# Kernel tuning notes

Hardware: AMD Instinct MI355X
Metric: run time of the kernel (lower is better)

## Reference

```python
import jax, jax.numpy as jnp
import numpy as np

B = 4096          # batch
F = 1024          # feature_count * embedding_dim
E = 16            # embedding_dim (domain embedding)
D = 8             # num_domains
T = F + E         # cross-net total dim
L = 3             # cross layers
EPS = 1e-5


def setup_inputs() -> dict:
    key = jax.random.key(0)
    ks = jax.random.split(key, 32)
    s = 0.02
    inp = {}
    inp["x"] = jax.random.normal(ks[0], (B, F), dtype=jnp.float32)
    inp["domain_ids"] = jax.random.randint(ks[1], (B,), 0, D)
    # partitioned normalization params
    inp["pn_weight"] = jnp.ones((D, F), jnp.float32)
    inp["pn_bias"] = jnp.zeros((D, F), jnp.float32)
    # domain embedding table
    inp["dom_emb"] = jax.random.normal(ks[2], (D, E), jnp.float32) * 0.1
    # cross network: L layers, each Linear(T->1, no bias) + additive bias vector
    inp["cross_w"] = jax.random.normal(ks[3], (L, T), jnp.float32) * s
    inp["cross_b"] = jnp.zeros((L, T), jnp.float32)
    # center MLP: T->512->256->128 (ReLU, ReLU, none)
    inp["cW1"] = jax.random.normal(ks[4], (T, 512), jnp.float32) * s
    inp["cb1"] = jnp.zeros((512,), jnp.float32)
    inp["cW2"] = jax.random.normal(ks[5], (512, 256), jnp.float32) * s
    inp["cb2"] = jnp.zeros((256,), jnp.float32)
    inp["cW3"] = jax.random.normal(ks[6], (256, 128), jnp.float32) * s
    inp["cb3"] = jnp.zeros((128,), jnp.float32)
    # per-domain nets: T->512->256->128; last bias initialized to domain_net_init_bias=1.0
    inp["dW1"] = jax.random.normal(ks[7], (D, T, 512), jnp.float32) * s
    inp["db1"] = jnp.zeros((D, 512), jnp.float32)
    inp["dW2"] = jax.random.normal(ks[8], (D, 512, 256), jnp.float32) * s
    inp["db2"] = jnp.zeros((D, 256), jnp.float32)
    inp["dW3"] = jax.random.normal(ks[9], (D, 256, 128), jnp.float32) * s
    inp["db3"] = jnp.ones((D, 128), jnp.float32)
    # final MLP: 128->64->1
    inp["fW1"] = jax.random.normal(ks[10], (128, 64), jnp.float32) * s
    inp["fb1"] = jnp.zeros((64,), jnp.float32)
    inp["fW2"] = jax.random.normal(ks[11], (64, 1), jnp.float32) * s
    inp["fb2"] = jnp.zeros((1,), jnp.float32)
    # auxiliary net: E->32->1
    inp["aW1"] = jax.random.normal(ks[12], (E, 32), jnp.float32) * s
    inp["ab1"] = jnp.zeros((32,), jnp.float32)
    inp["aW2"] = jax.random.normal(ks[13], (32, 1), jnp.float32) * s
    inp["ab2"] = jnp.zeros((1,), jnp.float32)
    return inp


def _forward(x, domain_ids, pn_weight, pn_bias, dom_emb, cross_w, cross_b,
             cW1, cb1, cW2, cb2, cW3, cb3,
             dW1, db1, dW2, db2, dW3, db3,
             fW1, fb1, fW2, fb2, aW1, ab1, aW2, ab2):
    # --- PartitionedNormalization: per-sample LayerNorm stats + domain-indexed affine ---
    mean = jnp.mean(x, axis=1, keepdims=True)
    var = jnp.mean((x - mean) ** 2, axis=1, keepdims=True)  # unbiased=False
    normed = (x - mean) / jnp.sqrt(var + EPS)
    normed = normed * pn_weight[domain_ids] + pn_bias[domain_ids]

    xd = dom_emb[domain_ids]                    # (B, E)
    x0 = jnp.concatenate([normed, xd], axis=1)  # (B, T)

    # --- CrossNetworkWithDomain ---
    xc = x0
    for i in range(L):
        proj = xc @ cross_w[i]                  # (B,)
        xc = x0 * proj[:, None] + cross_b[i] + xc

    # --- center MLP ---
    h = jax.nn.relu(xc @ cW1 + cb1)
    h = jax.nn.relu(h @ cW2 + cb2)
    h_center = h @ cW3 + cb3                    # (B, 128)

    # --- domain-specific nets: run all D nets, select per-sample ---
    a = jax.nn.relu(jnp.einsum('bi,dio->bdo', xc, dW1) + db1[None])   # (B, D, 512)
    a = jax.nn.relu(jnp.einsum('bdi,dio->bdo', a, dW2) + db2[None])   # (B, D, 256)
    a = jnp.einsum('bdi,dio->bdo', a, dW3) + db3[None]                # (B, D, 128)
    h_domain = a[jnp.arange(a.shape[0]), domain_ids]                  # (B, 128)

    # --- STAR fusion (tanh) ---
    fused = h_center * jnp.tanh(h_domain)

    # --- final MLP + auxiliary net ---
    main_logits = jax.nn.relu(fused @ fW1 + fb1) @ fW2 + fb2          # (B, 1)
    aux_logits = jax.nn.relu(xd @ aW1 + ab1) @ aW2 + ab2              # (B, 1)
    return jax.nn.sigmoid(main_logits + aux_logits)


def reference(x, domain_ids, pn_weight, pn_bias, dom_emb, cross_w, cross_b,
              cW1, cb1, cW2, cb2, cW3, cb3,
              dW1, db1, dW2, db2, dW3, db3,
              fW1, fb1, fW2, fb2, aW1, ab1, aW2, ab2):
    return _forward(x, domain_ids, pn_weight, pn_bias, dom_emb, cross_w, cross_b,
                    cW1, cb1, cW2, cb2, cW3, cb3,
                    dW1, db1, dW2, db2, dW3, db3,
                    fW1, fb1, fW2, fb2, aW1, ab1, aW2, ab2)
```

## Files before the change

### kernel.cpp

```cpp
#include <hip/hip_runtime.h>
#include <math.h>
#include <stdint.h>

#define BATCH 4096
#define FEAT  1024
#define EDIM  16
#define NDOM  8
#define TDIM  1040
#define KP1   1088
#define NLAYER 3
#define EPSV  1e-5f

typedef __attribute__((ext_vector_type(8))) short bf16x8;
typedef __attribute__((ext_vector_type(4))) float f32x4;

#define VMW(N)  __builtin_amdgcn_s_waitcnt((((N)&15)|(((N)>>4)<<14)|(15<<8)|(7<<4)))
#define LGKW0   __builtin_amdgcn_s_waitcnt((15|(3<<14)|(7<<4)))
#define SBAR    __builtin_amdgcn_s_barrier()
#define SCB     __builtin_amdgcn_sched_barrier(0)

__device__ __forceinline__ unsigned short f2bf(float f) {
    union { float f; unsigned int u; } v; v.f = f;
    unsigned int u = v.u;
    return (unsigned short)((u + 0x7fffu + ((u >> 16) & 1u)) >> 16);
}
__device__ __forceinline__ float bf2f(unsigned short u) {
    union { unsigned int u; float f; } v; v.u = ((unsigned int)u) << 16; return v.f;
}
__device__ __forceinline__ void gload_lds16(const void* g, void* l) {
    __builtin_amdgcn_global_load_lds(
        (const __attribute__((address_space(1))) void*)(g),
        (__attribute__((address_space(3))) void*)(l), 16, 0, 0);
}

#define T_W1 136
#define T_W2 32
#define T_W3 8
#define NCONV (T_W1*9 + T_W2*9 + T_W3*9)

__global__ __launch_bounds__(256) void front(
    const int* __restrict__ dom, int* __restrict__ perm, int* __restrict__ starts,
    const float* __restrict__ cW1, const float* __restrict__ dW1,
    const float* __restrict__ cW2, const float* __restrict__ dW2,
    const float* __restrict__ cW3, const float* __restrict__ dW3,
    unsigned short* __restrict__ Wc1b, unsigned short* __restrict__ Wd1b,
    unsigned short* __restrict__ Wc2b, unsigned short* __restrict__ Wd2b,
    unsigned short* __restrict__ Wc3b, unsigned short* __restrict__ Wd3b,
    const float* __restrict__ x,
    const float* __restrict__ pnw, const float* __restrict__ pnb,
    const float* __restrict__ demb,
    const float* __restrict__ crw, const float* __restrict__ crb,
    const float* __restrict__ aW1, const float* __restrict__ ab1,
    const float* __restrict__ aW2, const float* __restrict__ ab2,
    unsigned short* __restrict__ XCb, float* __restrict__ auxg) {
    int b = blockIdx.x;
    int t = threadIdx.x;

    if (b < NCONV) {
        __shared__ float tile[64][65];
        const float* src; unsigned short* dst; int K, N, Kp, rr;
        if (b < T_W1)            { src = cW1; dst = Wc1b; K = TDIM; N = 512; Kp = KP1; rr = b; }
        else if (b < T_W1*9)     { int r = b - T_W1; int z = r / T_W1; rr = r % T_W1;
                                   src = dW1 + (size_t)z * TDIM * 512; dst = Wd1b + (size_t)z * 512 * KP1;
                                   K = TDIM; N = 512; Kp = KP1; }
        else if (b < T_W1*9+T_W2)   { src = cW2; dst = Wc2b; K = 512; N = 256; Kp = 512; rr = b - T_W1*9; }
        else if (b < T_W1*9+T_W2*9) { int r = b - (T_W1*9+T_W2); int z = r / T_W2; rr = r % T_W2;
                                   src = dW2 + (size_t)z * 512 * 256; dst = Wd2b + (size_t)z * 256 * 512;
                                   K = 512; N = 256; Kp = 512; }
        else if (b < T_W1*9+T_W2*9+T_W3) { src = cW3; dst = Wc3b; K = 256; N = 128; Kp = 256; rr = b - (T_W1*9+T_W2*9); }
        else                     { int r = b - (T_W1*9+T_W2*9+T_W3); int z = r / T_W3; rr = r % T_W3;
                                   src = dW3 + (size_t)z * 256 * 128; dst = Wd3b + (size_t)z * 128 * 256;
                                   K = 256; N = 128; Kp = 256; }
        int kt = Kp >> 6;
        int kb = rr % kt, nb = rr / kt;
        int k0 = kb * 64, n0 = nb * 64;
        #pragma unroll
        for (int i = 0; i < 4; i++) {
            int flat = t + i * 256;
            int kr = flat >> 4, c4 = flat & 15;
            int k = k0 + kr;
            float4 v = make_float4(0.f, 0.f, 0.f, 0.f);
            if (k < K) v = *(const float4*)(src + (size_t)k * N + n0 + c4 * 4);
            tile[kr][c4 * 4 + 0] = v.x;
            tile[kr][c4 * 4 + 1] = v.y;
            tile[kr][c4 * 4 + 2] = v.z;
            tile[kr][c4 * 4 + 3] = v.w;
        }
        __syncthreads();
        #pragma unroll
        for (int i = 0; i < 4; i++) {
            int flat = t + i * 256;
            int n = flat >> 4, kg = flat & 15;
            ushort4 sv;
            sv.x = f2bf(tile[kg * 4 + 0][n]);
            sv.y = f2bf(tile[kg * 4 + 1][n]);
            sv.z = f2bf(tile[kg * 4 + 2][n]);
            sv.w = f2bf(tile[kg * 4 + 3][n]);
            *(ushort4*)(dst + (size_t)(n0 + n) * Kp + k0 + kg * 4) = sv;
        }
        return;
    }
    if (b == NCONV) {
        __shared__ int cnt[NDOM];
        __shared__ int off[NDOM];
        if (t < NDOM) cnt[t] = 0;
        __syncthreads();
        for (int i = t; i < BATCH; i += 256) atomicAdd(&cnt[dom[i]], 1);
        __syncthreads();
        if (t == 0) {
            int s = 0;
            for (int d = 0; d < NDOM; d++) { off[d] = s; starts[d] = s; s += cnt[d]; }
            starts[NDOM] = s;
        }
        __syncthreads();
        for (int i = t; i < BATCH; i += 256) {
            int p = atomicAdd(&off[dom[i]], 1);
            perm[p] = i;
        }
        return;
    }

    int w = t >> 6, lane = t & 63;
    int row = (b - NCONV - 1) * 4 + w;
    int d = dom[row];

    float4 X[4];
    #pragma unroll
    for (int j = 0; j < 4; j++)
        X[j] = *(const float4*)(x + (size_t)row * FEAT + 4 * lane + 256 * j);

    float s = 0.f, ss = 0.f;
    #pragma unroll
    for (int j = 0; j < 4; j++) {
        s  += X[j].x + X[j].y + X[j].z + X[j].w;
        ss += X[j].x*X[j].x + X[j].y*X[j].y + X[j].z*X[j].z + X[j].w*X[j].w;
    }
    #pragma unroll
    for (int m = 1; m < 64; m <<= 1) {
        s  += __shfl_xor(s,  m);
        ss += __shfl_xor(ss, m);
    }
    float mean = s / (float)FEAT;
    float var  = ss / (float)FEAT - mean * mean;
    float rstd = rsqrtf(var + EPSV);

    float4 x0[4], xc[4];
    #pragma unroll
    for (int j = 0; j < 4; j++) {
        float4 wv = *(const float4*)(pnw + (size_t)d * FEAT + 4 * lane + 256 * j);
        float4 bv = *(const float4*)(pnb + (size_t)d * FEAT + 4 * lane + 256 * j);
        x0[j].x = (X[j].x - mean) * rstd * wv.x + bv.x;
        x0[j].y = (X[j].y - mean) * rstd * wv.y + bv.y;
        x0[j].z = (X[j].z - mean) * rstd * wv.z + bv.z;
        x0[j].w = (X[j].w - mean) * rstd * wv.w + bv.w;
        xc[j] = x0[j];
    }
    float x0e = 0.f, xce = 0.f;
    if (lane < EDIM) { x0e = demb[d * EDIM + lane]; xce = x0e; }

    #pragma unroll
    for (int l = 0; l < NLAYER; l++) {
        const float* wl = crw + l * TDIM;
        const float* bl = crb + l * TDIM;
        float partial = 0.f;
        #pragma unroll
        for (int j = 0; j < 4; j++) {
            float4 wv = *(const float4*)(wl + 4 * lane + 256 * j);
            partial += xc[j].x*wv.x + xc[j].y*wv.y + xc[j].z*wv.z + xc[j].w*wv.w;
        }
        if (lane < EDIM) partial += xce * wl[FEAT + lane];
        #pragma unroll
        for (int m = 1; m < 64; m <<= 1) partial += __shfl_xor(partial, m);
        float proj = partial;
        #pragma unroll
        for (int j = 0; j < 4; j++) {
            float4 bv = *(const float4*)(bl + 4 * lane + 256 * j);
            xc[j].x = fmaf(x0[j].x, proj, bv.x + xc[j].x);
            xc[j].y = fmaf(x0[j].y, proj, bv.y + xc[j].y);
            xc[j].z = fmaf(x0[j].z, proj, bv.z + xc[j].z);
            xc[j].w = fmaf(x0[j].w, proj, bv.w + xc[j].w);
        }
        if (lane < EDIM) xce = fmaf(x0e, proj, bl[FEAT + lane] + xce);
    }

    #pragma unroll
    for (int j = 0; j < 4; j++) {
        ushort4 sv;
        sv.x = f2bf(xc[j].x); sv.y = f2bf(xc[j].y);
        sv.z = f2bf(xc[j].z); sv.w = f2bf(xc[j].w);
        *(ushort4*)(XCb + (size_t)row * KP1 + 4 * lane + 256 * j) = sv;
    }
    XCb[(size_t)row * KP1 + FEAT + lane] = (lane < EDIM) ? f2bf(xce) : 0;

    float h = (lane < 32) ? ab1[lane] : 0.f;
    #pragma unroll
    for (int e = 0; e < EDIM; e++) {
        float ev = __shfl(xce, e);
        if (lane < 32) h = fmaf(ev, aW1[e * 32 + lane], h);
    }
    float c = (lane < 32) ? fmaxf(h, 0.f) * aW2[lane] : 0.f;
    #pragma unroll
    for (int m = 1; m < 64; m <<= 1) c += __shfl_xor(c, m);
    if (lane == 0) auxg[row] = c + ab2[0];
}

__global__ __launch_bounds__(256) void gemm_l1_fused(
    const unsigned short* __restrict__ A,
    const unsigned short* __restrict__ Wc,
    const unsigned short* __restrict__ Wd,
    const float* __restrict__ bc, const float* __restrict__ bd,
    unsigned short* __restrict__ Cc, unsigned short* __restrict__ Cd,
    const int* __restrict__ starts, const int* __restrict__ perm) {
    __shared__ short As[2][64 * 64];
    __shared__ short Bs[2][128 * 64];

    int g = blockIdx.x;
    int d = 0, acc = 0, m0 = -1, mEnd = 0;
    #pragma unroll
    for (int dd = 0; dd < NDOM; dd++) {
        int c0 = starts[dd], c1 = starts[dd + 1];
        int ns = (c1 - c0 + 63) >> 6;
        if (m0 < 0 && g < acc + ns) { d = dd; m0 = c0 + ((g - acc) << 6); mEnd = c1; }
        acc += ns;
    }
    if (m0 < 0) return;
    int n0 = blockIdx.y * 64;

    int tid = threadIdx.x;
    int w = tid >> 6, lane = tid & 63;
    int lr = lane & 15, q = lane >> 4;

    const unsigned short* pA[2]; int sA[2];
    const unsigned short* pB[4]; int sB[4];
    #pragma unroll
    for (int i = 0; i < 2; i++) {
        int seg = i * 4 + w;
        int ch = seg * 64 + lane;
        int loc = ch >> 3, c = ch & 7;
        int mm = m0 + loc; if (mm > mEnd - 1) mm = mEnd - 1;
        int rowp = perm[mm];
        pA[i] = A + (size_t)rowp * KP1 + ((c ^ (loc & 7)) << 3);
        sA[i] = seg * 512;
    }
    #pragma unroll
    for (int i = 0; i < 4; i++) {
        int seg = i * 4 + w;
        int ch = seg * 64 + lane;
        int loc = ch >> 3, c = ch & 7;
        const unsigned short* base = (loc < 64)
            ? (Wc + (size_t)(n0 + loc) * KP1)
            : (Wd + ((size_t)d * 512 + n0 + (loc - 64)) * KP1);
        pB[i] = base + ((c ^ (loc & 7)) << 3);
        sB[i] = seg * 512;
    }

    f32x4 acc4[4][2];
    #pragma unroll
    for (int i = 0; i < 4; i++)
        #pragma unroll
        for (int j = 0; j < 2; j++)
            acc4[i][j] = (f32x4){0.f, 0.f, 0.f, 0.f};

    #pragma unroll
    for (int i = 0; i < 2; i++) gload_lds16(pA[i], As[0] + sA[i]);
    #pragma unroll
    for (int i = 0; i < 4; i++) gload_lds16(pB[i], Bs[0] + sB[i]);

    #pragma unroll 1
    for (int ks = 0; ks < KP1 / 64; ks++) {
        int cur = ks & 1, nxt = cur ^ 1;
        if (ks < KP1 / 64 - 1) {
            int k0 = (ks + 1) * 64;
            #pragma unroll
            for (int i = 0; i < 2; i++) gload_lds16(pA[i] + k0, As[nxt] + sA[i]);
            #pragma unroll
            for (int i = 0; i < 4; i++) gload_lds16(pB[i] + k0, Bs[nxt] + sB[i]);
            VMW(6);
        } else {
            VMW(0);
        }
        SBAR; SCB;
        #pragma unroll
        for (int half = 0; half < 2; half++) {
            int cc = half * 4 + q;
            bf16x8 af[4], bf[2];
            #pragma unroll
            for (int i = 0; i < 4; i++) {
                int m = i * 16 + lr;
                af[i] = *(const bf16x8*)(As[cur] + m * 64 + ((cc ^ (m & 7)) << 3));
            }
            #pragma unroll
            for (int j = 0; j < 2; j++) {
                int n = w * 32 + j * 16 + lr;
                bf[j] = *(const bf16x8*)(Bs[cur] + n * 64 + ((cc ^ (n & 7)) << 3));
            }
            #pragma unroll
            for (int i = 0; i < 4; i++)
                #pragma unroll
                for (int j = 0; j < 2; j++)
                    acc4[i][j] = __builtin_amdgcn_mfma_f32_16x16x32_bf16(
                        af[i], bf[j], acc4[i][j], 0, 0, 0);
        }
        LGKW0; SBAR; SCB;
    }

    int chain = w >> 1, hn = w & 1;
    const float* bias = chain ? (bd + d * 512) : bc;
    unsigned short* C = chain ? Cd : Cc;
    #pragma unroll
    for (int i = 0; i < 4; i++) {
        #pragma unroll
        for (int j = 0; j < 2; j++) {
            int col = n0 + hn * 32 + j * 16 + lr;
            float bvv = bias[col];
            int rowb = m0 + i * 16 + q * 4;
            #pragma unroll
            for (int r = 0; r < 4; r++) {
                int row = rowb + r;
                if (row >= mEnd) continue;
                C[(size_t)row * 512 + col] = f2bf(fmaxf(acc4[i][j][r] + bvv, 0.f));
            }
        }
    }
}

__global__ __launch_bounds__(256) void tail_fused(
    const unsigned short* __restrict__ H1c, const unsigned short* __restrict__ H1d,
    const unsigned short* __restrict__ Wc2, const unsigned short* __restrict__ Wd2,
    const float* __restrict__ cb2v, const float* __restrict__ db2v,
    const unsigned short* __restrict__ Wc3, const unsigned short* __restrict__ Wd3,
    const float* __restrict__ cb3v, const float* __restrict__ db3v,
    const float* __restrict__ fW1, const float* __restrict__ fb1,
    const float* __restrict__ fW2, const float* __restrict__ fb2,
    const float* __restrict__ auxg, const int* __restrict__ perm,
    const int* __restrict__ starts, float* __restrict__ out) {

    __shared__ __align__(16) char smem[98304];
    short* BufB[2]; short* BufA[2];
    #pragma unroll
    for (int i = 0; i < 2; i++) {
        BufB[i] = (short*)(smem + i * 36864);
        BufA[i] = (short*)(smem + i * 36864 + 32768);
    }
    short* H2    = (short*)(smem + 73728);
    short* fused = (short*)(smem + 90112);

    int g = blockIdx.x;
    int d = 0, acc = 0, m0 = -1, mEnd = 0;
    #pragma unroll
    for (int dd = 0; dd < NDOM; dd++) {
        int c0 = starts[dd], c1 = starts[dd + 1];
        int ns = (c1 - c0 + 31) >> 5;
        if (m0 < 0 && g < acc + ns) { d = dd; m0 = c0 + ((g - acc) << 5); mEnd = c1; }
        acc += ns;
    }
    if (m0 < 0) return;

    int tid = threadIdx.x;
    int w = tid >> 6, lane = tid & 63;
    int lr = lane & 15, q = lane >> 4;

    int bn = w * 8 + (lane >> 3);
    int sw = ((lane & 7) ^ (bn & 7)) << 3;
    int rowA = m0 + bn; if (rowA > mEnd - 1) rowA = mEnd - 1;

    const unsigned short* pA0  = H1c + (size_t)rowA * 512 + sw;
    const unsigned short* pA1  = H1d + (size_t)rowA * 512 + sw;
    const unsigned short* pW20 = Wc2 + (size_t)bn * 512 + sw;
    const unsigned short* pW21 = Wd2 + (size_t)d * 256 * 512 + (size_t)bn * 512 + sw;
    const unsigned short* pW30 = Wc3 + (size_t)bn * 256 + sw;
    const unsigned short* pW31 = Wd3 + (size_t)d * 128 * 256 + (size_t)bn * 256 + sw;

    auto istep = [&](int s) {
        int c = s / 12, k = s % 12, b = s & 1;
        if (k < 8) {
            const unsigned short* pa = c ? pA1 : pA0;
            const unsigned short* pw = c ? pW21 : pW20;
            int k0 = k * 64;
            gload_lds16(pa + k0, BufA[b] + w * 512);
            #pragma unroll
            for (int i = 0; i < 8; i++)
                gload_lds16(pw + (size_t)i * 32 * 512 + k0, BufB[b] + (i * 4 + w) * 512);
        } else {
            const unsigned short* pw = c ? pW31 : pW30;
            int k0 = (k - 8) * 64;
            #pragma unroll
            for (int i = 0; i < 4; i++)
                gload_lds16(pw + (size_t)i * 32 * 256 + k0, BufB[b] + (i * 4 + w) * 512);
        }
    };

    f32x4 acc2[2][4], acc3[2][2];

    auto cstep = [&](int s) {
        int c = s / 12, k = s % 12, b = s & 1;
        if (k < 8) {
            if (k == 0) {
                #pragma unroll
                for (int i = 0; i < 2; i++)
                    #pragma unroll
                    for (int j = 0; j < 4; j++) acc2[i][j] = (f32x4){0.f, 0.f, 0.f, 0.f};
            }
            #pragma unroll
            for (int half = 0; half < 2; half++) {
                int cc = half * 4 + q;
                bf16x8 af[2], bf[4];
                #pragma unroll
                for (int i = 0; i < 2; i++) {
                    int m = i * 16 + lr;
                    af[i] = *(const bf16x8*)(BufA[b] + m * 64 + ((cc ^ (m & 7)) << 3));
                }
                #pragma unroll
                for (int j = 0; j < 4; j++) {
                    int n = w * 64 + j * 16 + lr;
                    bf[j] = *(const bf16x8*)(BufB[b] + n * 64 + ((cc ^ (n & 7)) << 3));
                }
                #pragma unroll
                for (int i = 0; i < 2; i++)
                    #pragma unroll
                    for (int j = 0; j < 4; j++)
                        acc2[i][j] = __builtin_amdgcn_mfma_f32_16x16x32_bf16(
                            af[i], bf[j], acc2[i][j], 0, 0, 0);
            }
            if (k == 7) {
                const float* b2 = c ? (db2v + d * 256) : cb2v;
                #pragma unroll
                for (int i = 0; i < 2; i++)
                    #pragma unroll
                    for (int j = 0; j < 4; j++) {
                        int col = w * 64 + j * 16 + lr;
                        float bv = b2[col];
                        int cch = col >> 3;
                        #pragma unroll
                        for (int r = 0; r < 4; r++) {
                            int row = i * 16 + q * 4 + r;
                            int pc = (cch & 24) | ((cch ^ (row & 7)) & 7);
                            float v = fmaxf(acc2[i][j][r] + bv, 0.f);
                            H2[row * 256 + pc * 8 + (col & 7)] = (short)f2bf(v);
                        }
                    }
            }
        } else {
            int it = k - 8;
            if (it == 0) {
                #pragma unroll
                for (int i = 0; i < 2; i++)
                    #pragma unroll
                    for (int j = 0; j < 2; j++) acc3[i][j] = (f32x4){0.f, 0.f, 0.f, 0.f};
            }
            #pragma unroll
            for (int half = 0; half < 2; half++) {
                int cc = half * 4 + q;
                int C = it * 8 + cc;
                bf16x8 af[2], bf[2];
                #pragma unroll
                for (int i = 0; i < 2; i++) {
                    int m = i * 16 + lr;
                    int pcm = (C & 24) | ((C ^ (m & 7)) & 7);
                    af[i] = *(const bf16x8*)(H2 + m * 256 + pcm * 8);
                }
                #pragma unroll
                for (int j = 0; j < 2; j++) {
                    int n = w * 32 + j * 16 + lr;
                    bf[j] = *(const bf16x8*)(BufB[b] + n * 64 + ((cc ^ (n & 7)) << 3));
                }
                #pragma unroll
                for (int i = 0; i < 2; i++)
                    #pragma unroll
                    for (int j = 0; j < 2; j++)
                        acc3[i][j] = __builtin_amdgcn_mfma_f32_16x16x32_bf16(
                            af[i], bf[j], acc3[i][j], 0, 0, 0);
            }
            if (it == 3) {
                const float* b3 = c ? (db3v + d * 128) : cb3v;
                #pragma unroll
                for (int i = 0; i < 2; i++)
                    #pragma unroll
                    for (int j = 0; j < 2; j++) {
                        int col = w * 32 + j * 16 + lr;
                        float bv = b3[col];
                        int cch = col >> 3;
                        #pragma unroll
                        for (int r = 0; r < 4; r++) {
                            int row = i * 16 + q * 4 + r;
                            int pc = (cch & 8) | ((cch ^ (row & 7)) & 7);
                            int idx = row * 128 + pc * 8 + (col & 7);
                            if (c == 0) {
                                fused[idx] = (short)f2bf(acc3[i][j][r] + bv);
                            } else {
                                float cv = bf2f((unsigned short)fused[idx]);
                                fused[idx] = (short)f2bf(cv * tanhf(acc3[i][j][r] + bv));
                            }
                        }
                    }
            }
        }
    };

    #define TSTEP(S, NW) do { \
        VMW(NW); SBAR; SCB; \
        cstep(S); \
        LGKW0; SBAR; SCB; \
        if ((S) + 2 < 24) istep((S) + 2); \
    } while (0)

    istep(0); istep(1);

    TSTEP(0, 9);   TSTEP(1, 9);   TSTEP(2, 9);   TSTEP(3, 9);
    TSTEP(4, 9);   TSTEP(5, 9);   TSTEP(6, 9);   TSTEP(7, 4);
    TSTEP(8, 4);   TSTEP(9, 4);   TSTEP(10, 4);  TSTEP(11, 9);
    TSTEP(12, 9);  TSTEP(13, 9);  TSTEP(14, 9);  TSTEP(15, 9);
    TSTEP(16, 9);  TSTEP(17, 9);  TSTEP(18, 9);  TSTEP(19, 4);
    TSTEP(20, 4);  TSTEP(21, 4);  TSTEP(22, 4);  TSTEP(23, 0);
    #undef TSTEP

    __syncthreads();

    short* Bsf = BufB[0];
    float* Ls  = (float*)BufA[0];
    for (int s2 = tid; s2 < 1024; s2 += 256) {
        int n = s2 >> 4, cch = s2 & 15;
        bf16x8 vv;
        #pragma unroll
        for (int kk = 0; kk < 8; kk++)
            vv[kk] = (short)f2bf(fW1[(cch * 8 + kk) * 64 + n]);
        int pc = (cch & 8) | ((cch ^ (n & 7)) & 7);
        *(bf16x8*)(Bsf + n * 128 + pc * 8) = vv;
    }
    __syncthreads();

    int wm = w >> 1, wn = w & 1;
    f32x4 acc2f[2];
    #pragma unroll
    for (int j = 0; j < 2; j++) acc2f[j] = (f32x4){0.f, 0.f, 0.f, 0.f};
    #pragma unroll
    for (int g2 = 0; g2 < 4; g2++) {
        int cc = g2 * 4 + q;
        int m = wm * 16 + lr;
        int pcm = (cc & 8) | ((cc ^ (m & 7)) & 7);
        bf16x8 af = *(const bf16x8*)(fused + m * 128 + pcm * 8);
        #pragma unroll
        for (int j = 0; j < 2; j++) {
            int n = wn * 32 + j * 16 + lr;
            int pcn = (cc & 8) | ((cc ^ (n & 7)) & 7);
            bf16x8 bf = *(const bf16x8*)(Bsf + n * 128 + pcn * 8);
            acc2f[j] = __builtin_amdgcn_mfma_f32_16x16x32_bf16(af, bf, acc2f[j], 0, 0, 0);
        }
    }

    float w2v[2], b1v[2];
    #pragma unroll
    for (int j = 0; j < 2; j++) {
        int col = wn * 32 + j * 16 + lr;
        w2v[j] = fW2[col];
        b1v[j] = fb1[col];
    }
    float rowv[4];
    #pragma unroll
    for (int r = 0; r < 4; r++) {
        float v = 0.f;
        #pragma unroll
        for (int j = 0; j < 2; j++)
            v += fmaxf(acc2f[j][r] + b1v[j], 0.f) * w2v[j];
        v += __shfl_xor(v, 1);
        v += __shfl_xor(v, 2);
        v += __shfl_xor(v, 4);
        v += __shfl_xor(v, 8);
        rowv[r] = v;
    }
    if (wn == 0 && lr == 0) {
        #pragma unroll
        for (int r = 0; r < 4; r++)
            Ls[wm * 16 + q * 4 + r] = rowv[r];
    }
    __syncthreads();
    if (wn == 1 && lr == 0) {
        float b2 = fb2[0];
        #pragma unroll
        for (int r = 0; r < 4; r++) {
            int row = wm * 16 + q * 4 + r;
            int p = m0 + row;
            if (p < mEnd) {
                int orow = perm[p];
                float logit = Ls[row] + rowv[r] + b2 + auxg[orow];
                out[orow] = 1.f / (1.f + expf(-logit));
            }
        }
    }
}

extern "C" void kernel_launch(void* const* d_in, const int* in_sizes, int n_in,
                              void* d_out, int out_size, void* d_ws, size_t ws_size,
                              hipStream_t stream) {
    (void)in_sizes; (void)n_in; (void)out_size; (void)ws_size;

    const float* x    = (const float*)d_in[0];
    const int*   dom  = (const int*)  d_in[1];
    const float* pnw  = (const float*)d_in[2];
    const float* pnb  = (const float*)d_in[3];
    const float* demb = (const float*)d_in[4];
    const float* crw  = (const float*)d_in[5];
    const float* crb  = (const float*)d_in[6];
    const float* cW1  = (const float*)d_in[7];
    const float* cb1  = (const float*)d_in[8];
    const float* cW2  = (const float*)d_in[9];
    const float* cb2  = (const float*)d_in[10];
    const float* cW3  = (const float*)d_in[11];
    const float* cb3  = (const float*)d_in[12];
    const float* dW1  = (const float*)d_in[13];
    const float* db1  = (const float*)d_in[14];
    const float* dW2  = (const float*)d_in[15];
    const float* db2  = (const float*)d_in[16];
    const float* dW3  = (const float*)d_in[17];
    const float* db3  = (const float*)d_in[18];
    const float* fW1  = (const float*)d_in[19];
    const float* fb1  = (const float*)d_in[20];
    const float* fW2  = (const float*)d_in[21];
    const float* fb2  = (const float*)d_in[22];
    const float* aW1  = (const float*)d_in[23];
    const float* ab1  = (const float*)d_in[24];
    const float* aW2  = (const float*)d_in[25];
    const float* ab2  = (const float*)d_in[26];
    float* out = (float*)d_out;

    char* base = (char*)d_ws;
    size_t o = 0;
    auto alloc = [&](size_t bytes) { char* p = base + o; o += (bytes + 255) & ~size_t(255); return p; };

    int* perm   = (int*)alloc(BATCH * 4);
    int* starts = (int*)alloc((NDOM + 1) * 4);
    float* auxg = (float*)alloc(BATCH * 4);
    unsigned short* XCb  = (unsigned short*)alloc((size_t)BATCH * KP1 * 2);
    unsigned short* H1c  = (unsigned short*)alloc((size_t)BATCH * 512 * 2);
    unsigned short* H1d  = (unsigned short*)alloc((size_t)BATCH * 512 * 2);
    unsigned short* Wc1b = (unsigned short*)alloc((size_t)512 * KP1 * 2);
    unsigned short* Wd1b = (unsigned short*)alloc((size_t)NDOM * 512 * KP1 * 2);
    unsigned short* Wc2b = (unsigned short*)alloc((size_t)256 * 512 * 2);
    unsigned short* Wd2b = (unsigned short*)alloc((size_t)NDOM * 256 * 512 * 2);
    unsigned short* Wc3b = (unsigned short*)alloc((size_t)128 * 256 * 2);
    unsigned short* Wd3b = (unsigned short*)alloc((size_t)NDOM * 128 * 256 * 2);

    front<<<NCONV + 1 + BATCH / 4, 256, 0, stream>>>(
        dom, perm, starts, cW1, dW1, cW2, dW2, cW3, dW3,
        Wc1b, Wd1b, Wc2b, Wd2b, Wc3b, Wd3b,
        x, pnw, pnb, demb, crw, crb, aW1, ab1, aW2, ab2, XCb, auxg);

    gemm_l1_fused<<<dim3(72, 8), 256, 0, stream>>>(
        XCb, Wc1b, Wd1b, cb1, db1, H1c, H1d, starts, perm);

    tail_fused<<<136, 256, 0, stream>>>(
        H1c, H1d, Wc2b, Wd2b, cb2, db2, Wc3b, Wd3b, cb3, db3,
        fW1, fb1, fW2, fb2, auxg, perm, starts, out);
}
```

Before: 181.5 us.

## Split tail kernel into per-chain GEMM blocks plus separate final-MLP kernel

The fused tail kernel ran the center and domain layer-2/3 chains back to back in one block of 136. It now launches 272 blocks, one chain each, writing layer-3 outputs to global buffers. A new kernel then applies the tanh fusion and the final MLP over the permuted rows. This doubles parallelism for the tail GEMMs so more CUs are busy, at the cost of an extra launch and a global round trip of the layer-3 activations.

```diff
diff --git a/kernel.cpp b/kernel.cpp
--- a/kernel.cpp
+++ b/kernel.cpp
@@ -324,28 +324,26 @@
     }
 }
 
-__global__ __launch_bounds__(256) void tail_fused(
+__global__ __launch_bounds__(256) void tail_gemm(
     const unsigned short* __restrict__ H1c, const unsigned short* __restrict__ H1d,
     const unsigned short* __restrict__ Wc2, const unsigned short* __restrict__ Wd2,
     const float* __restrict__ cb2v, const float* __restrict__ db2v,
     const unsigned short* __restrict__ Wc3, const unsigned short* __restrict__ Wd3,
     const float* __restrict__ cb3v, const float* __restrict__ db3v,
-    const float* __restrict__ fW1, const float* __restrict__ fb1,
-    const float* __restrict__ fW2, const float* __restrict__ fb2,
-    const float* __restrict__ auxg, const int* __restrict__ perm,
-    const int* __restrict__ starts, float* __restrict__ out) {
-
-    __shared__ __align__(16) char smem[98304];
+    unsigned short* __restrict__ Hc3, unsigned short* __restrict__ Hd3,
+    const int* __restrict__ starts) {
+
+    __shared__ __align__(16) char smem[90112];
     short* BufB[2]; short* BufA[2];
     #pragma unroll
     for (int i = 0; i < 2; i++) {
         BufB[i] = (short*)(smem + i * 36864);
         BufA[i] = (short*)(smem + i * 36864 + 32768);
     }
-    short* H2    = (short*)(smem + 73728);
-    short* fused = (short*)(smem + 90112);
-
-    int g = blockIdx.x;
+    short* H2 = (short*)(smem + 73728);
+
+    int gb = blockIdx.x;
+    int chain = gb & 1, g = gb >> 1;
     int d = 0, acc = 0, m0 = -1, mEnd = 0;
     #pragma unroll
     for (int dd = 0; dd < NDOM; dd++) {
@@ -364,36 +362,35 @@
     int sw = ((lane & 7) ^ (bn & 7)) << 3;
     int rowA = m0 + bn; if (rowA > mEnd - 1) rowA = mEnd - 1;
 
-    const unsigned short* pA0  = H1c + (size_t)rowA * 512 + sw;
-    const unsigned short* pA1  = H1d + (size_t)rowA * 512 + sw;
-    const unsigned short* pW20 = Wc2 + (size_t)bn * 512 + sw;
-    const unsigned short* pW21 = Wd2 + (size_t)d * 256 * 512 + (size_t)bn * 512 + sw;
-    const unsigned short* pW30 = Wc3 + (size_t)bn * 256 + sw;
-    const unsigned short* pW31 = Wd3 + (size_t)d * 128 * 256 + (size_t)bn * 256 + sw;
+    const unsigned short* pA  = (chain ? H1d : H1c) + (size_t)rowA * 512 + sw;
+    const unsigned short* pW2 = (chain ? (Wd2 + (size_t)d * 256 * 512) : Wc2)
+                                + (size_t)bn * 512 + sw;
+    const unsigned short* pW3 = (chain ? (Wd3 + (size_t)d * 128 * 256) : Wc3)
+                                + (size_t)bn * 256 + sw;
+    const float* b2 = chain ? (db2v + d * 256) : cb2v;
+    const float* b3 = chain ? (db3v + d * 128) : cb3v;
+    unsigned short* G = chain ? Hd3 : Hc3;
 
     auto istep = [&](int s) {
-        int c = s / 12, k = s % 12, b = s & 1;
+        int k = s, b = s & 1;
         if (k < 8) {
-            const unsigned short* pa = c ? pA1 : pA0;
-            const unsigned short* pw = c ? pW21 : pW20;
             int k0 = k * 64;
-            gload_lds16(pa + k0, BufA[b] + w * 512);
+            gload_lds16(pA + k0, BufA[b] + w * 512);
             #pragma unroll
             for (int i = 0; i < 8; i++)
-                gload_lds16(pw + (size_t)i * 32 * 512 + k0, BufB[b] + (i * 4 + w) * 512);
+                gload_lds16(pW2 + (size_t)i * 32 * 512 + k0, BufB[b] + (i * 4 + w) * 512);
         } else {
-            const unsigned short* pw = c ? pW31 : pW30;
             int k0 = (k - 8) * 64;
             #pragma unroll
             for (int i = 0; i < 4; i++)
-                gload_lds16(pw + (size_t)i * 32 * 256 + k0, BufB[b] + (i * 4 + w) * 512);
+                gload_lds16(pW3 + (size_t)i * 32 * 256 + k0, BufB[b] + (i * 4 + w) * 512);
         }
     };
 
     f32x4 acc2[2][4], acc3[2][2];
 
     auto cstep = [&](int s) {
-        int c = s / 12, k = s % 12, b = s & 1;
+        int k = s, b = s & 1;
         if (k < 8) {
             if (k == 0) {
                 #pragma unroll
@@ -423,7 +420,6 @@
                             af[i], bf[j], acc2[i][j], 0, 0, 0);
             }
             if (k == 7) {
-                const float* b2 = c ? (db2v + d * 256) : cb2v;
                 #pragma unroll
                 for (int i = 0; i < 2; i++)
                     #pragma unroll
@@ -472,25 +468,18 @@
                             af[i], bf[j], acc3[i][j], 0, 0, 0);
             }
             if (it == 3) {
-                const float* b3 = c ? (db3v + d * 128) : cb3v;
                 #pragma unroll
                 for (int i = 0; i < 2; i++)
                     #pragma unroll
                     for (int j = 0; j < 2; j++) {
                         int col = w * 32 + j * 16 + lr;
                         float bv = b3[col];
-                        int cch = col >> 3;
                         #pragma unroll
                         for (int r = 0; r < 4; r++) {
                             int row = i * 16 + q * 4 + r;
-                            int pc = (cch & 8) | ((cch ^ (row & 7)) & 7);
-                            int idx = row * 128 + pc * 8 + (col & 7);
-                            if (c == 0) {
-                                fused[idx] = (short)f2bf(acc3[i][j][r] + bv);
-                            } else {
-                                float cv = bf2f((unsigned short)fused[idx]);
-                                fused[idx] = (short)f2bf(cv * tanhf(acc3[i][j][r] + bv));
-                            }
+                            int prow = m0 + row;
+                            if (prow < mEnd)
+                                G[(size_t)prow * 128 + col] = f2bf(acc3[i][j][r] + bv);
                         }
                     }
             }
@@ -501,23 +490,43 @@
         VMW(NW); SBAR; SCB; \
         cstep(S); \
         LGKW0; SBAR; SCB; \
-        if ((S) + 2 < 24) istep((S) + 2); \
+        if ((S) + 2 < 12) istep((S) + 2); \
     } while (0)
 
     istep(0); istep(1);
-
     TSTEP(0, 9);   TSTEP(1, 9);   TSTEP(2, 9);   TSTEP(3, 9);
     TSTEP(4, 9);   TSTEP(5, 9);   TSTEP(6, 9);   TSTEP(7, 4);
-    TSTEP(8, 4);   TSTEP(9, 4);   TSTEP(10, 4);  TSTEP(11, 9);
-    TSTEP(12, 9);  TSTEP(13, 9);  TSTEP(14, 9);  TSTEP(15, 9);
-    TSTEP(16, 9);  TSTEP(17, 9);  TSTEP(18, 9);  TSTEP(19, 4);
-    TSTEP(20, 4);  TSTEP(21, 4);  TSTEP(22, 4);  TSTEP(23, 0);
+    TSTEP(8, 4);   TSTEP(9, 4);   TSTEP(10, 4);  TSTEP(11, 0);
     #undef TSTEP
-
-    __syncthreads();
-
-    short* Bsf = BufB[0];
-    float* Ls  = (float*)BufA[0];
+}
+
+__global__ __launch_bounds__(256) void tail_final(
+    const unsigned short* __restrict__ Hc3, const unsigned short* __restrict__ Hd3,
+    const float* __restrict__ fW1, const float* __restrict__ fb1,
+    const float* __restrict__ fW2, const float* __restrict__ fb2,
+    const float* __restrict__ auxg, const int* __restrict__ perm,
+    float* __restrict__ out) {
+    __shared__ __align__(16) short fused[32 * 128];
+    __shared__ __align__(16) short Bsf[64 * 128];
+    __shared__ float Ls[32];
+
+    int m0 = blockIdx.x * 32;
+    int tid = threadIdx.x;
+    int w = tid >> 6, lane = tid & 63;
+    int lr = lane & 15, q = lane >> 4;
+
+    for (int s2 = tid; s2 < 512; s2 += 256) {
+        int row = s2 >> 4, cch = s2 & 15;
+        bf16x8 cv = *(const bf16x8*)(Hc3 + (size_t)(m0 + row) * 128 + cch * 8);
+        bf16x8 dv = *(const bf16x8*)(Hd3 + (size_t)(m0 + row) * 128 + cch * 8);
+        bf16x8 fv;
+        #pragma unroll
+        for (int kk = 0; kk < 8; kk++)
+            fv[kk] = (short)f2bf(bf2f((unsigned short)cv[kk]) *
+                                 tanhf(bf2f((unsigned short)dv[kk])));
+        int pc = (cch & 8) | ((cch ^ (row & 7)) & 7);
+        *(bf16x8*)(fused + row * 128 + pc * 8) = fv;
+    }
     for (int s2 = tid; s2 < 1024; s2 += 256) {
         int n = s2 >> 4, cch = s2 & 15;
         bf16x8 vv;
@@ -579,12 +588,9 @@
         #pragma unroll
         for (int r = 0; r < 4; r++) {
             int row = wm * 16 + q * 4 + r;
-            int p = m0 + row;
-            if (p < mEnd) {
-                int orow = perm[p];
-                float logit = Ls[row] + rowv[r] + b2 + auxg[orow];
-                out[orow] = 1.f / (1.f + expf(-logit));
-            }
+            int orow = perm[m0 + row];
+            float logit = Ls[row] + rowv[r] + b2 + auxg[orow];
+            out[orow] = 1.f / (1.f + expf(-logit));
         }
     }
 }
@@ -633,6 +639,8 @@
     unsigned short* XCb  = (unsigned short*)alloc((size_t)BATCH * KP1 * 2);
     unsigned short* H1c  = (unsigned short*)alloc((size_t)BATCH * 512 * 2);
     unsigned short* H1d  = (unsigned short*)alloc((size_t)BATCH * 512 * 2);
+    unsigned short* Hc3  = (unsigned short*)alloc((size_t)BATCH * 128 * 2);
+    unsigned short* Hd3  = (unsigned short*)alloc((size_t)BATCH * 128 * 2);
     unsigned short* Wc1b = (unsigned short*)alloc((size_t)512 * KP1 * 2);
     unsigned short* Wd1b = (unsigned short*)alloc((size_t)NDOM * 512 * KP1 * 2);
     unsigned short* Wc2b = (unsigned short*)alloc((size_t)256 * 512 * 2);
@@ -648,7 +656,10 @@
     gemm_l1_fused<<<dim3(72, 8), 256, 0, stream>>>(
         XCb, Wc1b, Wd1b, cb1, db1, H1c, H1d, starts, perm);
 
-    tail_fused<<<136, 256, 0, stream>>>(
+    tail_gemm<<<272, 256, 0, stream>>>(
         H1c, H1d, Wc2b, Wd2b, cb2, db2, Wc3b, Wd3b, cb3, db3,
-        fW1, fb1, fW2, fb2, auxg, perm, starts, out);
-}
+        Hc3, Hd3, starts);
+
+    tail_final<<<BATCH / 32, 256, 0, stream>>>(
+        Hc3, Hd3, fW1, fb1, fW2, fb2, auxg, perm, out);
+}
```

Measured after the change: 185.3 us. 1.02x slower.
